# Performance work log

Hardware: AMD Instinct MI355X
Metric: run time of the kernel (lower is better)

The kernel has to match this reference:

```python
import jax, jax.numpy as jnp
import numpy as np

D_K = 64


def setup_inputs() -> dict:
    key = jax.random.key(0)
    k1, k2, k3, k4 = jax.random.split(key, 4)
    B, Lq, Lk, d = 16, 2048, 2048, D_K
    q = jax.random.normal(k1, (B, Lq, d), dtype=jnp.float32)
    k = jax.random.normal(k2, (B, Lk, d), dtype=jnp.float32)
    v = jax.random.normal(k3, (B, Lk, d), dtype=jnp.float32)
    mask = jax.random.bernoulli(k4, 0.5, (B, Lq, Lk))  # bool, True = masked
    return {"q": q, "k": k, "v": v, "mask": mask}


def reference(q, k, v, mask):
    # Faithful to the torch module: scores -> masked_fill(mask, 0) BEFORE exp,
    # unstable exp (no max subtraction), sum-normalize, then AV.
    d_k = k.shape[-1]
    scores = jnp.einsum('bqd,bkd->bqk', q, k) / jnp.sqrt(jnp.float32(d_k))
    scores = jnp.where(mask, jnp.zeros((), dtype=scores.dtype), scores)
    e = jnp.exp(scores)                      # masked slots contribute exp(0)=1
    attn = e / jnp.sum(e, axis=-1, keepdims=True)
    # dropout is identity in eval mode
    return jnp.einsum('bqk,bkd->bqd', attn, v)
```

## Files before the change

kernel.cpp:

```cpp
#include <hip/hip_runtime.h>
#include <stdint.h>

namespace {

typedef _Float16 f16x8 __attribute__((ext_vector_type(8)));
typedef __fp16 fp16x2 __attribute__((ext_vector_type(2)));
typedef float f32x16 __attribute__((ext_vector_type(16)));
typedef unsigned short u16x4 __attribute__((ext_vector_type(4)));

constexpr int BATCH = 16;
constexpr int LQ = 2048;
constexpr int LK = 2048;
constexpr int DIM = 64;
constexpr float SCALE = 0.125f;

constexpr size_t WS_KF = 1ull << 20;
constexpr size_t WS_VT = 6ull << 20;

__device__ inline unsigned short f2h_bits(float x) {
  _Float16 h = (_Float16)x;
  union { _Float16 h; unsigned short u; } c;
  c.h = h;
  return c.u;
}
__device__ inline int cvt_pk_f16(float lo, float hi) {
  union { fp16x2 h2; int i; } u;
  u.h2 = __builtin_amdgcn_cvt_pkrtz(lo, hi);
  return u.i;
}


__global__ __launch_bounds__(256) void prep_kv(
    const float* __restrict__ kp, const float* __restrict__ vp,
    const uint32_t* __restrict__ maskp, int* __restrict__ flag,
    unsigned short* __restrict__ kf, unsigned short* __restrict__ vt) {
  const int blk = blockIdx.x;
  if (blk < 2048) {
    int idx = blk * 256 + threadIdx.x;
    int b = idx >> 15;
    int rem = idx & 32767;
    int r = rem >> 4;
    int d0 = (rem & 15) * 4;
    float4 kv = *(const float4*)(kp + ((size_t)b * LK + r) * DIM + d0);
    u16x4 hv;
#pragma unroll
    for (int j = 0; j < 4; ++j) hv[j] = f2h_bits((&kv.x)[j]);
    int T = r >> 6;
    int rin = r & 63;
    int f = rin >> 5;
    int m = rin & 31;
    int s = d0 >> 4;
    int hi = (d0 >> 3) & 1;
    int e0 = d0 & 7;
    size_t off =
        ((((size_t)(b * 32 + T) * 2 + f) * 4 + s) * 64 + (hi * 32 + m)) * 8 +
        e0;
    *(u16x4*)(kf + off) = hv;
  } else if (blk < 2560) {
    int idx = (blk - 2048) * 256 + threadIdx.x;
    int b = idx >> 13;
    int rem = idx & 8191;
    int kq = rem >> 4;
    int dq = rem & 15;
    int k0 = kq * 4;
    int T = k0 >> 6;
    int kin = k0 & 63;
    const float* vg = vp + ((size_t)b * LK + k0) * DIM + dq * 4;
    unsigned short tmp[4][4];
#pragma unroll
    for (int j = 0; j < 4; ++j) {
      float4 vf = *(const float4*)(vg + j * DIM);
#pragma unroll
      for (int i2 = 0; i2 < 4; ++i2) tmp[j][i2] = f2h_bits((&vf.x)[i2]);
    }
    int ks = kin >> 4;
    int hi = (kin >> 3) & 1;
    int e0 = kin & 7;
#pragma unroll
    for (int j2 = 0; j2 < 4; ++j2) {
      int d = dq * 4 + j2;
      int nb = d >> 5;
      u16x4 od = {tmp[0][j2], tmp[1][j2], tmp[2][j2], tmp[3][j2]};
      size_t off = ((((size_t)(b * 32 + T) * 2 + nb) * 4 + ks) * 64 +
                    (hi * 32 + (d & 31))) * 8 + e0;
      *(u16x4*)(vt + off) = od;
    }
  } else {
    __shared__ int bad;
    if (threadIdx.x == 0) bad = 0;
    __syncthreads();
    int my = 0;
    for (int i = threadIdx.x; i < 4096; i += 256) {
      uint32_t w = maskp[i];
      if (w > 1u && w != 0x3F800000u) my = 1;
    }
    if (my) atomicOr(&bad, 1);
    __syncthreads();
    if (threadIdx.x == 0) *flag = bad;
  }
}

__global__ __launch_bounds__(256, 2) void attn_mfma(
    const float* __restrict__ qp, const unsigned short* __restrict__ kf_g,
    const unsigned short* __restrict__ vt_g,
    const uint32_t* __restrict__ maskp, const int* __restrict__ flagp,
    float* __restrict__ out) {
  __shared__ __align__(16) unsigned char arena[3 * 64 * 33 * 4];
  __shared__ float den_s[32];
  unsigned char* NB = arena;
  float* X = (float*)arena;

  const int tid = threadIdx.x;
  const int h = tid >> 6;
  const int l = tid & 63;
  const int m31 = l & 31;
  const int hi = l >> 5;
  const int xcd = blockIdx.x & 7;
  const int idx = blockIdx.x >> 3;
  const int b = xcd * 2 + (idx >> 6);
  const int qbase = (idx & 63) * 32;
  const int qrow = qbase + m31;
  const int isU8 = *flagp;

  {
    const size_t mbase = ((size_t)b * LQ + qbase) * LK;
    if (!isU8) {
      const uint32_t* mg = maskp + mbase;
      for (int i = 0; i < 32; ++i) {
        const int u = i * 256 + tid;
        const uint32_t* src = mg + (size_t)u * 8;
        uint4 x0 = *(const uint4*)(src);
        uint4 x1 = *(const uint4*)(src + 4);
        unsigned bits =
            (unsigned)(x0.x != 0u) | ((unsigned)(x0.y != 0u) << 1) |
            ((unsigned)(x0.z != 0u) << 2) | ((unsigned)(x0.w != 0u) << 3) |
            ((unsigned)(x1.x != 0u) << 4) | ((unsigned)(x1.y != 0u) << 5) |
            ((unsigned)(x1.z != 0u) << 6) | ((unsigned)(x1.w != 0u) << 7);
        const int row = u >> 8;
        const int T = (u >> 3) & 31;
        const int e2 = u & 7;
        NB[(T * 32 + row) * 8 + e2] = (unsigned char)bits;
      }
    } else {
      const uint8_t* mg = (const uint8_t*)maskp + mbase;
      for (int i = 0; i < 8; ++i) {
        const int c = i * 256 + tid;
        const uint8_t* src = mg + (size_t)c * 32;
        uint4 x0 = *(const uint4*)(src);
        uint4 x1 = *(const uint4*)(src + 16);
        uint32_t w32 = 0;
#pragma unroll
        for (int q = 0; q < 4; ++q) {
          uint32_t w0 = (&x0.x)[q], w1 = (&x1.x)[q];
          uint32_t nib0 = (unsigned)((w0 & 0xFFu) != 0u) |
                          ((unsigned)(((w0 >> 8) & 0xFFu) != 0u) << 1) |
                          ((unsigned)(((w0 >> 16) & 0xFFu) != 0u) << 2) |
                          ((unsigned)(((w0 >> 24) & 0xFFu) != 0u) << 3);
          uint32_t nib1 = (unsigned)((w1 & 0xFFu) != 0u) |
                          ((unsigned)(((w1 >> 8) & 0xFFu) != 0u) << 1) |
                          ((unsigned)(((w1 >> 16) & 0xFFu) != 0u) << 2) |
                          ((unsigned)(((w1 >> 24) & 0xFFu) != 0u) << 3);
          w32 |= (nib0 << (q * 4)) | (nib1 << (16 + q * 4));
        }
        const int u0 = c * 4;
        const int row = u0 >> 8;
        const int T = (u0 >> 3) & 31;
        const int e2 = u0 & 7;
        *(uint32_t*)&NB[(T * 32 + row) * 8 + e2] = w32;
      }
    }
  }
  __syncthreads();

  const unsigned short* kb =
      kf_g + (size_t)(b * 32 + h * 8) * 4096 + (size_t)l * 8;
  const unsigned short* vb =
      vt_g + (size_t)(b * 32 + h * 8) * 4096 + (size_t)l * 8;

  f16x8 qf[4];
  {
    const float* qr = qp + ((size_t)b * LQ + qrow) * DIM;
#pragma unroll
    for (int s = 0; s < 4; ++s) {
#pragma unroll
      for (int j2 = 0; j2 < 2; ++j2) {
        float4 x = *(const float4*)(qr + s * 16 + hi * 8 + j2 * 4);
#pragma unroll
        for (int j = 0; j < 4; ++j) qf[s][j2 * 4 + j] = (_Float16)(&x.x)[j];
      }
    }
  }

  f32x16 oA = (f32x16)(0.f), oB = (f32x16)(0.f);
  float denA = 0.f, denB = 0.f;

  f16x8 kc0[4], kc1[4];
  f16x8 vb0[4], vb1[4];

#pragma unroll
  for (int s = 0; s < 4; ++s) {
    kc0[s] = *(const f16x8*)(kb + s * 512);
    kc1[s] = *(const f16x8*)(kb + 2048 + s * 512);
  }

  for (int t = 0; t < 8; ++t) {
    const size_t tb = (size_t)t * 4096;
    const unsigned long long mb =
        *(const unsigned long long*)&NB[((h * 8 + t) * 32 + m31) * 8];
    const uint32_t mb0 = (uint32_t)mb;
    const uint32_t mb1 = (uint32_t)(mb >> 32);
#pragma unroll
    for (int s = 0; s < 4; ++s) {
      vb0[s] = *(const f16x8*)(vb + tb + s * 512);
      vb1[s] = *(const f16x8*)(vb + tb + 2048 + s * 512);
    }

    f32x16 sA = (f32x16)(0.f), sB = (f32x16)(0.f);
    __builtin_amdgcn_s_setprio(1);
#pragma unroll
    for (int s = 0; s < 4; ++s) {
      sA = __builtin_amdgcn_mfma_f32_32x32x16_f16(kc0[s], qf[s], sA, 0, 0, 0);
      sB = __builtin_amdgcn_mfma_f32_32x32x16_f16(kc1[s], qf[s], sB, 0, 0, 0);
    }
    __builtin_amdgcn_s_setprio(0);

    if (t < 7) {
#pragma unroll
      for (int s = 0; s < 4; ++s) {
        kc0[s] = *(const f16x8*)(kb + tb + 4096 + s * 512);
        kc1[s] = *(const f16x8*)(kb + tb + 4096 + 2048 + s * 512);
      }
    }

    const int hi4 = hi * 4;
#pragma unroll
    for (int reg = 0; reg < 16; ++reg) {
      const int crow = (reg & 3) + 8 * (reg >> 2);
      float eA = ((mb0 >> (crow + hi4)) & 1u) ? 1.0f : __expf(sA[reg] * SCALE);
      float eB = ((mb1 >> (crow + hi4)) & 1u) ? 1.0f : __expf(sB[reg] * SCALE);
      denA += eA;
      denB += eB;
      sA[reg] = eA;
      sB[reg] = eB;
    }

#define PV_STEP(SV, A_, KS_)                                                \
  do {                                                                      \
    int c0x = cvt_pk_f16(SV[8 * A_ + 0], SV[8 * A_ + 1]);                   \
    int c1x = cvt_pk_f16(SV[8 * A_ + 2], SV[8 * A_ + 3]);                   \
    int c0y = cvt_pk_f16(SV[8 * A_ + 4], SV[8 * A_ + 5]);                   \
    int c1y = cvt_pk_f16(SV[8 * A_ + 6], SV[8 * A_ + 7]);                   \
    asm("v_permlane32_swap_b32 %0, %1" : "+v"(c0x), "+v"(c0y));             \
    asm("v_permlane32_swap_b32 %0, %1" : "+v"(c1x), "+v"(c1y));             \
    union { int d[4]; f16x8 v; } pa_;                                       \
    pa_.d[0] = c0x; pa_.d[1] = c1x; pa_.d[2] = c0y; pa_.d[3] = c1y;         \
    oA = __builtin_amdgcn_mfma_f32_32x32x16_f16(pa_.v, vb0[KS_], oA, 0, 0,  \
                                                0);                         \
    oB = __builtin_amdgcn_mfma_f32_32x32x16_f16(pa_.v, vb1[KS_], oB, 0, 0,  \
                                                0);                         \
  } while (0)

    __builtin_amdgcn_s_setprio(1);
    PV_STEP(sA, 0, 0);
    PV_STEP(sA, 1, 1);
    PV_STEP(sB, 0, 2);
    PV_STEP(sB, 1, 3);
    __builtin_amdgcn_s_setprio(0);
#undef PV_STEP
  }

  float den = denA + denB;
  __syncthreads();
  if (h > 0) {
    float* xp = X + ((size_t)((h - 1) * 64 + l)) * 33;
#pragma unroll
    for (int reg = 0; reg < 16; ++reg) {
      xp[reg] = oA[reg];
      xp[16 + reg] = oB[reg];
    }
    xp[32] = den;
  }
  __syncthreads();
  if (h == 0) {
#pragma unroll
    for (int p = 0; p < 3; ++p) {
      const float* xp = X + ((size_t)(p * 64 + l)) * 33;
#pragma unroll
      for (int reg = 0; reg < 16; ++reg) {
        oA[reg] += xp[reg];
        oB[reg] += xp[16 + reg];
      }
      den += xp[32];
    }
    den += __shfl_xor(den, 32);
    if (l < 32) den_s[m31] = 1.0f / den;
    float* ob = out + ((size_t)b * LQ + qbase) * DIM;
#pragma unroll
    for (int reg = 0; reg < 16; ++reg) {
      const int qr2 = (reg & 3) + 8 * (reg >> 2) + hi * 4;
      const float inv = den_s[qr2];
      ob[qr2 * DIM + m31] = oA[reg] * inv;
      ob[qr2 * DIM + 32 + m31] = oB[reg] * inv;
    }
  }
}

}

extern "C" void kernel_launch(void* const* d_in, const int* in_sizes, int n_in,
                              void* d_out, int out_size, void* d_ws,
                              size_t ws_size, hipStream_t stream) {
  const float* q = (const float*)d_in[0];
  const float* k = (const float*)d_in[1];
  const float* v = (const float*)d_in[2];
  const uint32_t* mask = (const uint32_t*)d_in[3];
  float* out = (float*)d_out;
  int* flag = (int*)d_ws;
  unsigned short* kf_g = (unsigned short*)((char*)d_ws + WS_KF);
  unsigned short* vt_g = (unsigned short*)((char*)d_ws + WS_VT);

  prep_kv<<<2561, 256, 0, stream>>>(k, v, mask, flag, kf_g, vt_g);
  attn_mfma<<<dim3(1024), 256, 0, stream>>>(q, kf_g, vt_g, mask, flag, out);
}
```

Measured before the change: 83.20 us.

## Process two query tiles per block, prefetching second tile's mask during compute

Each block now handles 64 query rows as two 32-row groups, halving the grid to 512 blocks. While computing the first group, it loads and bit-packs the second group's mask into a second LDS buffer, overlapping the mask stream with the MFMA work. This hides the mask read latency that was previously exposed before compute. The costs are less parallelism across the GPU, more registers held live for the in-flight mask loads, and a larger LDS footprint.

```diff
diff --git a/kernel.cpp b/kernel.cpp
--- a/kernel.cpp
+++ b/kernel.cpp
@@ -27,6 +27,29 @@
   union { fp16x2 h2; int i; } u;
   u.h2 = __builtin_amdgcn_cvt_pkrtz(lo, hi);
   return u.i;
+}
+__device__ inline unsigned pack8(uint4 x0, uint4 x1) {
+  return (unsigned)(x0.x != 0u) | ((unsigned)(x0.y != 0u) << 1) |
+         ((unsigned)(x0.z != 0u) << 2) | ((unsigned)(x0.w != 0u) << 3) |
+         ((unsigned)(x1.x != 0u) << 4) | ((unsigned)(x1.y != 0u) << 5) |
+         ((unsigned)(x1.z != 0u) << 6) | ((unsigned)(x1.w != 0u) << 7);
+}
+__device__ inline uint32_t pack32u8(uint4 x0, uint4 x1) {
+  uint32_t w32 = 0;
+#pragma unroll
+  for (int q = 0; q < 4; ++q) {
+    uint32_t w0 = (&x0.x)[q], w1 = (&x1.x)[q];
+    uint32_t nib0 = (unsigned)((w0 & 0xFFu) != 0u) |
+                    ((unsigned)(((w0 >> 8) & 0xFFu) != 0u) << 1) |
+                    ((unsigned)(((w0 >> 16) & 0xFFu) != 0u) << 2) |
+                    ((unsigned)(((w0 >> 24) & 0xFFu) != 0u) << 3);
+    uint32_t nib1 = (unsigned)((w1 & 0xFFu) != 0u) |
+                    ((unsigned)(((w1 >> 8) & 0xFFu) != 0u) << 1) |
+                    ((unsigned)(((w1 >> 16) & 0xFFu) != 0u) << 2) |
+                    ((unsigned)(((w1 >> 24) & 0xFFu) != 0u) << 3);
+    w32 |= (nib0 << (q * 4)) | (nib1 << (16 + q * 4));
+  }
+  return w32;
 }
 
 
@@ -105,10 +128,9 @@
     const unsigned short* __restrict__ vt_g,
     const uint32_t* __restrict__ maskp, const int* __restrict__ flagp,
     float* __restrict__ out) {
-  __shared__ __align__(16) unsigned char arena[3 * 64 * 33 * 4];
+  __shared__ __align__(16) unsigned char NB[2][8192];
+  __shared__ __align__(16) float X[3 * 64 * 33];
   __shared__ float den_s[32];
-  unsigned char* NB = arena;
-  float* X = (float*)arena;
 
   const int tid = threadIdx.x;
   const int h = tid >> 6;
@@ -117,56 +139,34 @@
   const int hi = l >> 5;
   const int xcd = blockIdx.x & 7;
   const int idx = blockIdx.x >> 3;
-  const int b = xcd * 2 + (idx >> 6);
-  const int qbase = (idx & 63) * 32;
-  const int qrow = qbase + m31;
+  const int b = xcd * 2 + (idx >> 5);
+  const int qb64 = (idx & 31) * 64;
   const int isU8 = *flagp;
 
   {
-    const size_t mbase = ((size_t)b * LQ + qbase) * LK;
+    const size_t mbase = ((size_t)b * LQ + qb64) * LK;
     if (!isU8) {
       const uint32_t* mg = maskp + mbase;
+#pragma unroll 4
       for (int i = 0; i < 32; ++i) {
         const int u = i * 256 + tid;
         const uint32_t* src = mg + (size_t)u * 8;
         uint4 x0 = *(const uint4*)(src);
         uint4 x1 = *(const uint4*)(src + 4);
-        unsigned bits =
-            (unsigned)(x0.x != 0u) | ((unsigned)(x0.y != 0u) << 1) |
-            ((unsigned)(x0.z != 0u) << 2) | ((unsigned)(x0.w != 0u) << 3) |
-            ((unsigned)(x1.x != 0u) << 4) | ((unsigned)(x1.y != 0u) << 5) |
-            ((unsigned)(x1.z != 0u) << 6) | ((unsigned)(x1.w != 0u) << 7);
-        const int row = u >> 8;
-        const int T = (u >> 3) & 31;
-        const int e2 = u & 7;
-        NB[(T * 32 + row) * 8 + e2] = (unsigned char)bits;
+        NB[0][(((u >> 3) & 31) * 32 + (u >> 8)) * 8 + (u & 7)] =
+            (unsigned char)pack8(x0, x1);
       }
     } else {
       const uint8_t* mg = (const uint8_t*)maskp + mbase;
+#pragma unroll 4
       for (int i = 0; i < 8; ++i) {
         const int c = i * 256 + tid;
         const uint8_t* src = mg + (size_t)c * 32;
         uint4 x0 = *(const uint4*)(src);
         uint4 x1 = *(const uint4*)(src + 16);
-        uint32_t w32 = 0;
-#pragma unroll
-        for (int q = 0; q < 4; ++q) {
-          uint32_t w0 = (&x0.x)[q], w1 = (&x1.x)[q];
-          uint32_t nib0 = (unsigned)((w0 & 0xFFu) != 0u) |
-                          ((unsigned)(((w0 >> 8) & 0xFFu) != 0u) << 1) |
-                          ((unsigned)(((w0 >> 16) & 0xFFu) != 0u) << 2) |
-                          ((unsigned)(((w0 >> 24) & 0xFFu) != 0u) << 3);
-          uint32_t nib1 = (unsigned)((w1 & 0xFFu) != 0u) |
-                          ((unsigned)(((w1 >> 8) & 0xFFu) != 0u) << 1) |
-                          ((unsigned)(((w1 >> 16) & 0xFFu) != 0u) << 2) |
-                          ((unsigned)(((w1 >> 24) & 0xFFu) != 0u) << 3);
-          w32 |= (nib0 << (q * 4)) | (nib1 << (16 + q * 4));
-        }
         const int u0 = c * 4;
-        const int row = u0 >> 8;
-        const int T = (u0 >> 3) & 31;
-        const int e2 = u0 & 7;
-        *(uint32_t*)&NB[(T * 32 + row) * 8 + e2] = w32;
+        *(uint32_t*)&NB[0][(((u0 >> 3) & 31) * 32 + (u0 >> 8)) * 8 +
+                           (u0 & 7)] = pack32u8(x0, x1);
       }
     }
   }
@@ -174,75 +174,102 @@
 
   const unsigned short* kb =
       kf_g + (size_t)(b * 32 + h * 8) * 4096 + (size_t)l * 8;
-  const unsigned short* vb =
+  const unsigned short* vbp =
       vt_g + (size_t)(b * 32 + h * 8) * 4096 + (size_t)l * 8;
-
-  f16x8 qf[4];
-  {
-    const float* qr = qp + ((size_t)b * LQ + qrow) * DIM;
+  const size_t mbaseB = ((size_t)b * LQ + qb64 + 32) * LK;
+  const uint32_t* mgB32 = maskp + mbaseB;
+  const uint8_t* mgB8 = (const uint8_t*)maskp + mbaseB;
+
+  for (int g = 0; g < 2; ++g) {
+    const int qrow = qb64 + g * 32 + m31;
+
+    f16x8 qf[4];
+    {
+      const float* qr = qp + ((size_t)b * LQ + qrow) * DIM;
+#pragma unroll
+      for (int s = 0; s < 4; ++s) {
+#pragma unroll
+        for (int j2 = 0; j2 < 2; ++j2) {
+          float4 x = *(const float4*)(qr + s * 16 + hi * 8 + j2 * 4);
+#pragma unroll
+          for (int j = 0; j < 4; ++j) qf[s][j2 * 4 + j] = (_Float16)(&x.x)[j];
+        }
+      }
+    }
+
+    f32x16 oA = (f32x16)(0.f), oB = (f32x16)(0.f);
+    float denA = 0.f, denB = 0.f;
+    f16x8 kc0[4], kc1[4], vb0[4], vb1[4];
+
 #pragma unroll
     for (int s = 0; s < 4; ++s) {
-#pragma unroll
-      for (int j2 = 0; j2 < 2; ++j2) {
-        float4 x = *(const float4*)(qr + s * 16 + hi * 8 + j2 * 4);
-#pragma unroll
-        for (int j = 0; j < 4; ++j) qf[s][j2 * 4 + j] = (_Float16)(&x.x)[j];
-      }
-    }
-  }
-
-  f32x16 oA = (f32x16)(0.f), oB = (f32x16)(0.f);
-  float denA = 0.f, denB = 0.f;
-
-  f16x8 kc0[4], kc1[4];
-  f16x8 vb0[4], vb1[4];
-
-#pragma unroll
-  for (int s = 0; s < 4; ++s) {
-    kc0[s] = *(const f16x8*)(kb + s * 512);
-    kc1[s] = *(const f16x8*)(kb + 2048 + s * 512);
-  }
-
-  for (int t = 0; t < 8; ++t) {
-    const size_t tb = (size_t)t * 4096;
-    const unsigned long long mb =
-        *(const unsigned long long*)&NB[((h * 8 + t) * 32 + m31) * 8];
-    const uint32_t mb0 = (uint32_t)mb;
-    const uint32_t mb1 = (uint32_t)(mb >> 32);
-#pragma unroll
-    for (int s = 0; s < 4; ++s) {
-      vb0[s] = *(const f16x8*)(vb + tb + s * 512);
-      vb1[s] = *(const f16x8*)(vb + tb + 2048 + s * 512);
-    }
-
-    f32x16 sA = (f32x16)(0.f), sB = (f32x16)(0.f);
-    __builtin_amdgcn_s_setprio(1);
-#pragma unroll
-    for (int s = 0; s < 4; ++s) {
-      sA = __builtin_amdgcn_mfma_f32_32x32x16_f16(kc0[s], qf[s], sA, 0, 0, 0);
-      sB = __builtin_amdgcn_mfma_f32_32x32x16_f16(kc1[s], qf[s], sB, 0, 0, 0);
-    }
-    __builtin_amdgcn_s_setprio(0);
-
-    if (t < 7) {
+      kc0[s] = *(const f16x8*)(kb + s * 512);
+      kc1[s] = *(const f16x8*)(kb + 2048 + s * 512);
+    }
+
+    for (int t = 0; t < 8; ++t) {
+      const size_t tb = (size_t)t * 4096;
+
+      uint4 s0, s1, s2, s3, s4, s5, s6, s7;
+      if (g == 0) {
+        if (!isU8) {
+          const int u_ = t * 1024 + tid;
+          s0 = *(const uint4*)(mgB32 + (size_t)u_ * 8);
+          s1 = *(const uint4*)(mgB32 + (size_t)u_ * 8 + 4);
+          s2 = *(const uint4*)(mgB32 + (size_t)(u_ + 256) * 8);
+          s3 = *(const uint4*)(mgB32 + (size_t)(u_ + 256) * 8 + 4);
+          s4 = *(const uint4*)(mgB32 + (size_t)(u_ + 512) * 8);
+          s5 = *(const uint4*)(mgB32 + (size_t)(u_ + 512) * 8 + 4);
+          s6 = *(const uint4*)(mgB32 + (size_t)(u_ + 768) * 8);
+          s7 = *(const uint4*)(mgB32 + (size_t)(u_ + 768) * 8 + 4);
+        } else {
+          const int c_ = t * 256 + tid;
+          s0 = *(const uint4*)(mgB8 + (size_t)c_ * 32);
+          s1 = *(const uint4*)(mgB8 + (size_t)c_ * 32 + 16);
+        }
+      }
+
+      const unsigned long long mb =
+          *(const unsigned long long*)&NB[g][((h * 8 + t) * 32 + m31) * 8];
+      const uint32_t mb0 = (uint32_t)mb;
+      const uint32_t mb1 = (uint32_t)(mb >> 32);
+
 #pragma unroll
       for (int s = 0; s < 4; ++s) {
-        kc0[s] = *(const f16x8*)(kb + tb + 4096 + s * 512);
-        kc1[s] = *(const f16x8*)(kb + tb + 4096 + 2048 + s * 512);
-      }
-    }
-
-    const int hi4 = hi * 4;
-#pragma unroll
-    for (int reg = 0; reg < 16; ++reg) {
-      const int crow = (reg & 3) + 8 * (reg >> 2);
-      float eA = ((mb0 >> (crow + hi4)) & 1u) ? 1.0f : __expf(sA[reg] * SCALE);
-      float eB = ((mb1 >> (crow + hi4)) & 1u) ? 1.0f : __expf(sB[reg] * SCALE);
-      denA += eA;
-      denB += eB;
-      sA[reg] = eA;
-      sB[reg] = eB;
-    }
+        vb0[s] = *(const f16x8*)(vbp + tb + s * 512);
+        vb1[s] = *(const f16x8*)(vbp + tb + 2048 + s * 512);
+      }
+
+      f32x16 sA = (f32x16)(0.f), sB = (f32x16)(0.f);
+      __builtin_amdgcn_s_setprio(1);
+#pragma unroll
+      for (int s = 0; s < 4; ++s) {
+        sA = __builtin_amdgcn_mfma_f32_32x32x16_f16(kc0[s], qf[s], sA, 0, 0, 0);
+        sB = __builtin_amdgcn_mfma_f32_32x32x16_f16(kc1[s], qf[s], sB, 0, 0, 0);
+      }
+      __builtin_amdgcn_s_setprio(0);
+
+      if (t < 7) {
+#pragma unroll
+        for (int s = 0; s < 4; ++s) {
+          kc0[s] = *(const f16x8*)(kb + tb + 4096 + s * 512);
+          kc1[s] = *(const f16x8*)(kb + tb + 4096 + 2048 + s * 512);
+        }
+      }
+
+      const int hi4 = hi * 4;
+#pragma unroll
+      for (int reg = 0; reg < 16; ++reg) {
+        const int crow = (reg & 3) + 8 * (reg >> 2);
+        float eA =
+            ((mb0 >> (crow + hi4)) & 1u) ? 1.0f : __expf(sA[reg] * SCALE);
+        float eB =
+            ((mb1 >> (crow + hi4)) & 1u) ? 1.0f : __expf(sB[reg] * SCALE);
+        denA += eA;
+        denB += eB;
+        sA[reg] = eA;
+        sB[reg] = eB;
+      }
 
 #define PV_STEP(SV, A_, KS_)                                                \
   do {                                                                      \
@@ -260,47 +287,67 @@
                                                 0);                         \
   } while (0)
 
-    __builtin_amdgcn_s_setprio(1);
-    PV_STEP(sA, 0, 0);
-    PV_STEP(sA, 1, 1);
-    PV_STEP(sB, 0, 2);
-    PV_STEP(sB, 1, 3);
-    __builtin_amdgcn_s_setprio(0);
+      __builtin_amdgcn_s_setprio(1);
+      PV_STEP(sA, 0, 0);
+      PV_STEP(sA, 1, 1);
+      PV_STEP(sB, 0, 2);
+      PV_STEP(sB, 1, 3);
+      __builtin_amdgcn_s_setprio(0);
 #undef PV_STEP
-  }
-
-  float den = denA + denB;
-  __syncthreads();
-  if (h > 0) {
-    float* xp = X + ((size_t)((h - 1) * 64 + l)) * 33;
-#pragma unroll
-    for (int reg = 0; reg < 16; ++reg) {
-      xp[reg] = oA[reg];
-      xp[16 + reg] = oB[reg];
-    }
-    xp[32] = den;
-  }
-  __syncthreads();
-  if (h == 0) {
-#pragma unroll
-    for (int p = 0; p < 3; ++p) {
-      const float* xp = X + ((size_t)(p * 64 + l)) * 33;
+
+      if (g == 0) {
+        if (!isU8) {
+          const int u_ = t * 1024 + tid;
+#define WRB(SS0, SS1, UU)                                              \
+  NB[1][((((UU) >> 3) & 31) * 32 + ((UU) >> 8)) * 8 + ((UU) & 7)] =    \
+      (unsigned char)pack8(SS0, SS1)
+          WRB(s0, s1, u_);
+          WRB(s2, s3, u_ + 256);
+          WRB(s4, s5, u_ + 512);
+          WRB(s6, s7, u_ + 768);
+#undef WRB
+        } else {
+          const int c_ = t * 256 + tid;
+          const int u0 = c_ * 4;
+          *(uint32_t*)&NB[1][(((u0 >> 3) & 31) * 32 + (u0 >> 8)) * 8 +
+                             (u0 & 7)] = pack32u8(s0, s1);
+        }
+      }
+    }
+
+    float den = denA + denB;
+    __syncthreads();
+    if (h > 0) {
+      float* xp = X + ((size_t)((h - 1) * 64 + l)) * 33;
 #pragma unroll
       for (int reg = 0; reg < 16; ++reg) {
-        oA[reg] += xp[reg];
-        oB[reg] += xp[16 + reg];
-      }
-      den += xp[32];
-    }
-    den += __shfl_xor(den, 32);
-    if (l < 32) den_s[m31] = 1.0f / den;
-    float* ob = out + ((size_t)b * LQ + qbase) * DIM;
-#pragma unroll
-    for (int reg = 0; reg < 16; ++reg) {
-      const int qr2 = (reg & 3) + 8 * (reg >> 2) + hi * 4;
-      const float inv = den_s[qr2];
-      ob[qr2 * DIM + m31] = oA[reg] * inv;
-      ob[qr2 * DIM + 32 + m31] = oB[reg] * inv;
+        xp[reg] = oA[reg];
+        xp[16 + reg] = oB[reg];
+      }
+      xp[32] = den;
+    }
+    __syncthreads();
+    if (h == 0) {
+#pragma unroll
+      for (int p = 0; p < 3; ++p) {
+        const float* xp = X + ((size_t)(p * 64 + l)) * 33;
+#pragma unroll
+        for (int reg = 0; reg < 16; ++reg) {
+          oA[reg] += xp[reg];
+          oB[reg] += xp[16 + reg];
+        }
+        den += xp[32];
+      }
+      den += __shfl_xor(den, 32);
+      if (l < 32) den_s[m31] = 1.0f / den;
+      float* ob = out + ((size_t)b * LQ + qb64 + g * 32) * DIM;
+#pragma unroll
+      for (int reg = 0; reg < 16; ++reg) {
+        const int qr2 = (reg & 3) + 8 * (reg >> 2) + hi * 4;
+        const float inv = den_s[qr2];
+        ob[qr2 * DIM + m31] = oA[reg] * inv;
+        ob[qr2 * DIM + 32 + m31] = oB[reg] * inv;
+      }
     }
   }
 }
@@ -320,5 +367,5 @@
   unsigned short* vt_g = (unsigned short*)((char*)d_ws + WS_VT);
 
   prep_kv<<<2561, 256, 0, stream>>>(k, v, mask, flag, kf_g, vt_g);
-  attn_mfma<<<dim3(1024), 256, 0, stream>>>(q, kf_g, vt_g, mask, flag, out);
-}
+  attn_mfma<<<dim3(512), 256, 0, stream>>>(q, kf_g, vt_g, mask, flag, out);
+}
```

Result: slower. 136.3 us (+63.8%).
